# Optimization experiments

Hardware: AMD Instinct MI355X
Metric: run time of the kernel (lower is better)

## Reference

```python
import jax, jax.numpy as jnp
import numpy as np

PH = 512          # possible_hidden_units
PA = 512          # possible_activation_functions
NOUT = PH + PA    # n_outputs
H = 24            # n_hidden (hard-coded in module)
L = 32            # layer_limit
B = 8192          # batch_size


def setup_inputs() -> dict:
    key = jax.random.key(0)
    ks = jax.random.split(key, 7)
    k = 1.0 / np.sqrt(H).astype(np.float32)
    uni = lambda kk, sh: jax.random.uniform(kk, sh, jnp.float32, -k, k)
    return {
        "w_ih": uni(ks[0], (4 * H, NOUT)),
        "w_hh": uni(ks[1], (4 * H, H)),
        "b_ih": uni(ks[2], (4 * H,)),
        "b_hh": uni(ks[3], (4 * H,)),
        "w_lin": uni(ks[4], (NOUT, H)),
        "b_lin": uni(ks[5], (NOUT,)),
        # per-step uniforms for categorical inverse-CDF sampling (np.random.rand in torch)
        "u": jax.random.uniform(ks[6], (L, B), jnp.float32),
        "batch_size": B,
        "training": 1,
    }


def reference(w_ih, w_hh, b_ih, b_hh, w_lin, b_lin, u, batch_size, training):
    dtype = w_ih.dtype
    # alternating masks: even step -> hidden-unit actions, odd step -> activation actions
    base = jnp.arange(NOUT)
    mask_even = (base < PH).astype(dtype)
    mask_odd = (base >= PH).astype(dtype)
    parity = (jnp.arange(L) % 2)[:, None]
    masks = jnp.where(parity == 0, mask_even[None, :], mask_odd[None, :])  # [L, NOUT]

    train = bool(training)

    def step(carry, xs):
        h, c, a = carry            # h,c: [B,H]; a: one-hot [B,NOUT]
        mask, u_t = xs             # mask: [NOUT], u_t: [B]
        gates = a @ w_ih.T + b_ih + h @ w_hh.T + b_hh   # [B, 4H]
        ig, fg, gg, og = jnp.split(gates, 4, axis=1)
        i = jax.nn.sigmoid(ig)
        f = jax.nn.sigmoid(fg)
        g = jnp.tanh(gg)
        o = jax.nn.sigmoid(og)
        c = f * c + i * g
        h = o * jnp.tanh(c)
        out = jax.nn.softmax(h @ w_lin.T + b_lin, axis=1) * mask  # [B, NOUT]
        out = out / jnp.sum(out, axis=1, keepdims=True)
        if train:
            action = jnp.argmax(jnp.cumsum(out, axis=1) > u_t[:, None], axis=1)
        else:
            action = jnp.argmax(out, axis=1)
        p = jnp.take_along_axis(out, action[:, None], axis=1)[:, 0]  # [B]
        a_next = jax.nn.one_hot(action, NOUT, dtype=dtype)
        return (h, c, a_next), (p, action)

    init = (
        jnp.zeros((B, H), dtype),
        jnp.zeros((B, H), dtype),
        jnp.zeros((B, NOUT), dtype),
    )
    _, (probs, actions) = jax.lax.scan(step, init, (masks, u))
    # scan stacks along leading (step) axis -> transpose to [B, L]
    return probs.T, actions.T
```

## Files before the change

### kernel.cpp

```cpp
#include <hip/hip_runtime.h>
#include <math.h>

#define NOUTK 1024
#define PHK   512
#define HID   24
#define G4    96
#define LSTEPS 32
#define BATCH 8192
#define EPB   16

struct SmemD {
  float  stg[HID][128][8];
  float  whhT[HID][G4];
  float  blin[NOUTK];
  float  bihs[G4], bhhs[G4];
  double hsh[EPB][25];
  double scrM[8][EPB];
  double scrS[8][EPB];
  double candr[8][EPB];
  double tots[8][EPB];
  double r0sh[EPB];
  float  ubuf[LSTEPS][EPB];
  int    candj[8][EPB];
  int    actsh[EPB];
};

__device__ __forceinline__ float bf2f(unsigned short v) {
  union { unsigned u; float f; } x; x.u = ((unsigned)v) << 16; return x.f;
}
__device__ __forceinline__ unsigned short f2bf(float f) {
  unsigned u = __float_as_uint(f);
  unsigned r = 0x7FFFu + ((u >> 16) & 1u);
  return (unsigned short)((u + r) >> 16);
}
__device__ __forceinline__ float bfsnap(float f) { return bf2f(f2bf(f)); }

__global__ void __launch_bounds__(256)
transpose_wih(const float* __restrict__ wihf, float* __restrict__ wihT) {
  const int idx = blockIdx.x * 256 + threadIdx.x;
  const int j = idx / G4;
  const int r = idx - j * G4;
  wihT[idx] = wihf[r * NOUTK + j];
}

__global__ void __launch_bounds__(1024)
policy_kernel(const float* __restrict__ wihf,  const float* __restrict__ whhf,
              const float* __restrict__ bihf,  const float* __restrict__ bhhf,
              const float* __restrict__ wlinf, const float* __restrict__ blinf,
              const float* __restrict__ uf,    const float* __restrict__ wT,
              float* __restrict__ outg) {
  extern __shared__ char smraw[];
  SmemD* sm = (SmemD*)smraw;
  const int tid  = threadIdx.x;
  const int wave = tid >> 6;
  const int lane = tid & 63;
  const int s    = wave & 7;
  const int eg   = (wave >> 3) << 3;
  const int le   = lane & 7;
  const int jl   = lane >> 3;
  const int eG   = eg + le;
  const int geL  = blockIdx.x * EPB + wave;
  const int jgl0 = s * 64 + jl * 8;

  {
    const float4* row4 = (const float4*)(wlinf + tid * HID);
    #pragma unroll
    for (int q = 0; q < 6; ++q) {
      const float4 v = row4[q];
      sm->stg[q * 4 + 0][tid >> 3][tid & 7] = v.x;
      sm->stg[q * 4 + 1][tid >> 3][tid & 7] = v.y;
      sm->stg[q * 4 + 2][tid >> 3][tid & 7] = v.z;
      sm->stg[q * 4 + 3][tid >> 3][tid & 7] = v.w;
    }
  }
  for (int i = tid; i < G4 * HID; i += 1024) {
    const int row = i / HID, k = i % HID;
    sm->whhT[k][row] = whhf[i];
  }
  sm->blin[tid] = blinf[tid];
  if (tid < G4) { sm->bihs[tid] = bihf[tid]; sm->bhhs[tid] = bhhf[tid]; }
  if (tid < EPB * 25) ((double*)sm->hsh)[tid] = 0.0;
  if (tid < EPB) sm->actsh[tid] = -1;
  if (tid < LSTEPS * EPB) {
    const int t = tid >> 4, e = tid & 15;
    sm->ubuf[t][e] = uf[t * BATCH + blockIdx.x * EPB + e];
  }

  double creg = 0.0;
  __syncthreads();

  for (int t = 0; t < LSTEPS; ++t) {
    const int odd  = t & 1;
    const int base = odd ? PHK : 0;
    const int c    = (base >> 3) + s * 8 + jl;

    if (wave < 8 && (lane & 31) < HID) {
      const int eL = (wave << 1) + (lane >> 5);
      const int rl = lane & 31;
      const int a  = sm->actsh[eL];
      double g0, g1, g2, g3;
#define GATE(Q, GOUT)                                                        \
      { const int row = (Q) * HID + rl;                                      \
        const double colA = (a >= 0)                                         \
            ? (double)(wT ? wT[a * G4 + row] : wihf[row * NOUTK + a])        \
            : 0.0;                                                           \
        double mv = 0.0;                                                     \
        _Pragma("unroll 4")                                                  \
        for (int k = 0; k < HID; ++k)                                        \
          mv = fma(sm->hsh[eL][k], (double)sm->whhT[k][row], mv);            \
        GOUT = ((colA + (double)sm->bihs[row]) + mv) + (double)sm->bhhs[row]; \
        __builtin_amdgcn_sched_barrier(0); }
      GATE(0, g0) GATE(1, g1) GATE(2, g2) GATE(3, g3)
#undef GATE
      const double ig = 1.0 / (1.0 + exp(-g0));
      const double fg = 1.0 / (1.0 + exp(-g1));
      const double gv = tanh(g2);
      const double og = 1.0 / (1.0 + exp(-g3));
      creg = fg * creg + ig * gv;
      sm->hsh[eL][rl] = og * tanh(creg);
    }
    __syncthreads();

    double z0 = 0.0, z1 = 0.0, z2 = 0.0, z3 = 0.0,
           z4 = 0.0, z5 = 0.0, z6 = 0.0, z7 = 0.0;
    #pragma unroll 2
    for (int k = 0; k < HID; ++k) {
      const double hv = sm->hsh[eG][k];
      const float4 wa = *(const float4*)&sm->stg[k][c][0];
      const float4 wb = *(const float4*)&sm->stg[k][c][4];
      z0 = fma(hv, (double)wa.x, z0); z1 = fma(hv, (double)wa.y, z1);
      z2 = fma(hv, (double)wa.z, z2); z3 = fma(hv, (double)wa.w, z3);
      z4 = fma(hv, (double)wb.x, z4); z5 = fma(hv, (double)wb.y, z5);
      z6 = fma(hv, (double)wb.z, z6); z7 = fma(hv, (double)wb.w, z7);
    }
    {
      const float4 ba = *(const float4*)&sm->blin[base + jgl0];
      const float4 bb = *(const float4*)&sm->blin[base + jgl0 + 4];
      z0 += (double)ba.x; z1 += (double)ba.y; z2 += (double)ba.z; z3 += (double)ba.w;
      z4 += (double)bb.x; z5 += (double)bb.y; z6 += (double)bb.z; z7 += (double)bb.w;
    }

    double pm = fmax(fmax(fmax(z0, z1), fmax(z2, z3)),
                     fmax(fmax(z4, z5), fmax(z6, z7)));
    pm = fmax(pm, __shfl_xor(pm, 8));
    pm = fmax(pm, __shfl_xor(pm, 16));
    pm = fmax(pm, __shfl_xor(pm, 32));
    if (jl == 0) sm->scrM[s][eG] = pm;
    __syncthreads();
    double Me;
    {
      const double s0 = sm->scrM[0][eG], s1 = sm->scrM[1][eG],
                   s2 = sm->scrM[2][eG], s3 = sm->scrM[3][eG],
                   s4 = sm->scrM[4][eG], s5 = sm->scrM[5][eG],
                   s6 = sm->scrM[6][eG], s7 = sm->scrM[7][eG];
      Me = fmax(fmax(fmax(s0, s1), fmax(s2, s3)),
                fmax(fmax(s4, s5), fmax(s6, s7)));
    }

    z0 = exp(z0 - Me); z1 = exp(z1 - Me);
    __builtin_amdgcn_sched_barrier(0);
    z2 = exp(z2 - Me); z3 = exp(z3 - Me);
    __builtin_amdgcn_sched_barrier(0);
    z4 = exp(z4 - Me); z5 = exp(z5 - Me);
    __builtin_amdgcn_sched_barrier(0);
    z6 = exp(z6 - Me); z7 = exp(z7 - Me);
    double ps = ((((((z0 + z1) + z2) + z3) + z4) + z5) + z6) + z7;
    ps += __shfl_xor(ps, 8);
    ps += __shfl_xor(ps, 16);
    ps += __shfl_xor(ps, 32);
    if (jl == 0) sm->scrS[s][eG] = ps;
    __syncthreads();
    double inv;
    {
      const double s0 = sm->scrS[0][eG], s1 = sm->scrS[1][eG],
                   s2 = sm->scrS[2][eG], s3 = sm->scrS[3][eG],
                   s4 = sm->scrS[4][eG], s5 = sm->scrS[5][eG],
                   s6 = sm->scrS[6][eG], s7 = sm->scrS[7][eG];
      inv = 1.0 / (((s0 + s1) + (s2 + s3)) + ((s4 + s5) + (s6 + s7)));
    }

    const double p0 = z0 * inv,      p1 = p0 + z1 * inv,
                 p2 = p1 + z2 * inv, p3 = p2 + z3 * inv;
    const double p4 = p3 + z4 * inv, p5 = p4 + z5 * inv,
                 p6 = p5 + z6 * inv, p7 = p6 + z7 * inv;
    double exbase = 0.0, acc = 0.0;
    #pragma unroll
    for (int q2 = 0; q2 < 8; ++q2) {
      const double tq = __shfl(p7, q2 * 8 + le);
      if (q2 == jl) exbase = acc;
      acc += tq;
    }
    if (jl == 0) sm->tots[s][eG] = acc;
    if (s == 0 && lane < 8) sm->r0sh[eG] = p0;
    __syncthreads();

    double sb = exbase;
    for (int i = 0; i < s; ++i) sb += sm->tots[i][eG];
    const double ue = (double)sm->ubuf[t][eG];
    int jloc = 0x7FFFFFFF; double rsel = 0.0;
#define CROSS(R, PR, PRM1)                                                   \
    { const double C = sb + PR;                                              \
      if (jloc == 0x7FFFFFFF && C > ue) {                                    \
        jloc = jgl0 + (R); rsel = ((R) == 0) ? (PR) : ((PR) - (PRM1)); } }
    CROSS(0, p0, p0) CROSS(1, p1, p0) CROSS(2, p2, p1) CROSS(3, p3, p2)
    CROSS(4, p4, p3) CROSS(5, p5, p4) CROSS(6, p6, p5) CROSS(7, p7, p6)
#undef CROSS
    { int oj = __shfl_xor(jloc, 8);  double orr = __shfl_xor(rsel, 8);  if (oj < jloc) { jloc = oj; rsel = orr; } }
    { int oj = __shfl_xor(jloc, 16); double orr = __shfl_xor(rsel, 16); if (oj < jloc) { jloc = oj; rsel = orr; } }
    { int oj = __shfl_xor(jloc, 32); double orr = __shfl_xor(rsel, 32); if (oj < jloc) { jloc = oj; rsel = orr; } }
    if (jl == 0) { sm->candj[s][eG] = jloc; sm->candr[s][eG] = rsel; }
    __syncthreads();

    if (lane < 8) {
      int cj = sm->candj[lane][wave]; double cr = sm->candr[lane][wave];
      { int oj = __shfl_xor(cj, 1); double orr = __shfl_xor(cr, 1); if (oj < cj) { cj = oj; cr = orr; } }
      { int oj = __shfl_xor(cj, 2); double orr = __shfl_xor(cr, 2); if (oj < cj) { cj = oj; cr = orr; } }
      { int oj = __shfl_xor(cj, 4); double orr = __shfl_xor(cr, 4); if (oj < cj) { cj = oj; cr = orr; } }
      if (lane == 0) {
        int actg; double p;
        if (cj == 0x7FFFFFFF) {
          actg = 0;
          p = odd ? 0.0 : sm->r0sh[wave];
        } else {
          actg = base + cj; p = cr;
        }
        sm->actsh[wave] = actg;
        const int io = geL * LSTEPS + t;
        outg[io]                  = bfsnap((float)p);
        outg[BATCH * LSTEPS + io] = bfsnap((float)actg);
      }
    }
  }
}

extern "C" void kernel_launch(void* const* d_in, const int* in_sizes, int n_in,
                              void* d_out, int out_size, void* d_ws, size_t ws_size,
                              hipStream_t stream) {
  (void)in_sizes; (void)n_in; (void)out_size;
  const float* wT = nullptr;
  if (ws_size >= (size_t)(NOUTK * G4 * sizeof(float))) {
    transpose_wih<<<(NOUTK * G4) / 256, 256, 0, stream>>>(
        (const float*)d_in[0], (float*)d_ws);
    wT = (const float*)d_ws;
  }
  hipFuncSetAttribute((const void*)policy_kernel,
                      hipFuncAttributeMaxDynamicSharedMemorySize,
                      (int)sizeof(SmemD));
  policy_kernel<<<BATCH / EPB, 1024, sizeof(SmemD), stream>>>(
      (const float*)d_in[0], (const float*)d_in[1], (const float*)d_in[2],
      (const float*)d_in[3], (const float*)d_in[4], (const float*)d_in[5],
      (const float*)d_in[6], wT, (float*)d_out);
}
```

Measured before the change: 884.0 us.

## Stream transposed output weights from global memory instead of large shared staging

Adds a prep step that writes both the transposed input weights and a k-major transposed copy of the output projection weights into workspace. A new main kernel reads the output weights straight from global memory (through cache) with float4 loads, replacing the large per-block shared staging buffer. This shrinks shared memory per block so more blocks can be resident per CU, in exchange for repeated global/L2 reads of the weights at every step. The old kernel is kept as a fallback when the workspace is too small.

```diff
diff --git a/kernel.cpp b/kernel.cpp
--- a/kernel.cpp
+++ b/kernel.cpp
@@ -8,6 +8,21 @@
 #define LSTEPS 32
 #define BATCH 8192
 #define EPB   16
+
+struct SmemS {
+  float  whhT[HID][G4];
+  float  blin[NOUTK];
+  float  bihs[G4], bhhs[G4];
+  double hsh[EPB][25];
+  double scrM[8][EPB];
+  double scrS[8][EPB];
+  double candr[8][EPB];
+  double tots[8][EPB];
+  double r0sh[EPB];
+  float  ubuf[LSTEPS][EPB];
+  int    candj[8][EPB];
+  int    actsh[EPB];
+};
 
 struct SmemD {
   float  stg[HID][128][8];
@@ -36,19 +51,204 @@
 __device__ __forceinline__ float bfsnap(float f) { return bf2f(f2bf(f)); }
 
 __global__ void __launch_bounds__(256)
-transpose_wih(const float* __restrict__ wihf, float* __restrict__ wihT) {
+prep_ws(const float* __restrict__ wihf, const float* __restrict__ wlinf,
+        float* __restrict__ ws, int total) {
   const int idx = blockIdx.x * 256 + threadIdx.x;
-  const int j = idx / G4;
-  const int r = idx - j * G4;
-  wihT[idx] = wihf[r * NOUTK + j];
+  if (idx >= total) return;
+  if (idx < NOUTK * G4) {
+    const int j = idx / G4;
+    const int r = idx - j * G4;
+    ws[idx] = wihf[r * NOUTK + j];
+  } else {
+    const int i2  = idx - NOUTK * G4;
+    const int k   = i2 >> 10;
+    const int col = i2 & (NOUTK - 1);
+    ws[idx] = wlinf[col * HID + k];
+  }
+}
+
+__global__ void __launch_bounds__(1024, 8)
+policy_g(const float* __restrict__ whhf,  const float* __restrict__ bihf,
+         const float* __restrict__ bhhf,  const float* __restrict__ blinf,
+         const float* __restrict__ uf,    const float* __restrict__ wT,
+         const float* __restrict__ wKC,   float* __restrict__ outg) {
+  __shared__ SmemS smS;
+  SmemS* sm = &smS;
+  const int tid  = threadIdx.x;
+  const int wave = tid >> 6;
+  const int lane = tid & 63;
+  const int s    = wave & 7;
+  const int eg   = (wave >> 3) << 3;
+  const int le   = lane & 7;
+  const int jl   = lane >> 3;
+  const int eG   = eg + le;
+  const int geL  = blockIdx.x * EPB + wave;
+  const int jgl0 = s * 64 + jl * 8;
+
+  for (int i = tid; i < G4 * HID; i += 1024) {
+    const int row = i / HID, k = i % HID;
+    sm->whhT[k][row] = whhf[i];
+  }
+  sm->blin[tid] = blinf[tid];
+  if (tid < G4) { sm->bihs[tid] = bihf[tid]; sm->bhhs[tid] = bhhf[tid]; }
+  if (tid < EPB * 25) ((double*)sm->hsh)[tid] = 0.0;
+  if (tid < EPB) sm->actsh[tid] = -1;
+  if (tid < LSTEPS * EPB) {
+    const int t = tid >> 4, e = tid & 15;
+    sm->ubuf[t][e] = uf[t * BATCH + blockIdx.x * EPB + e];
+  }
+
+  double creg = 0.0;
+  __syncthreads();
+
+  for (int t = 0; t < LSTEPS; ++t) {
+    const int odd  = t & 1;
+    const int base = odd ? PHK : 0;
+
+    if (wave < 8 && (lane & 31) < HID) {
+      const int eL = (wave << 1) + (lane >> 5);
+      const int rl = lane & 31;
+      const int a  = sm->actsh[eL];
+      double g0, g1, g2, g3;
+#define GATE(Q, GOUT)                                                        \
+      { const int row = (Q) * HID + rl;                                      \
+        const double colA = (a >= 0) ? (double)wT[a * G4 + row] : 0.0;       \
+        double mv = 0.0;                                                     \
+        _Pragma("unroll 4")                                                  \
+        for (int k = 0; k < HID; ++k)                                        \
+          mv = fma(sm->hsh[eL][k], (double)sm->whhT[k][row], mv);            \
+        GOUT = ((colA + (double)sm->bihs[row]) + mv) + (double)sm->bhhs[row]; \
+        __builtin_amdgcn_sched_barrier(0); }
+      GATE(0, g0) GATE(1, g1) GATE(2, g2) GATE(3, g3)
+#undef GATE
+      const double ig = 1.0 / (1.0 + exp(-g0));
+      const double fg = 1.0 / (1.0 + exp(-g1));
+      const double gv = tanh(g2);
+      const double og = 1.0 / (1.0 + exp(-g3));
+      creg = fg * creg + ig * gv;
+      sm->hsh[eL][rl] = og * tanh(creg);
+    }
+    __syncthreads();
+
+    double z0 = 0.0, z1 = 0.0, z2 = 0.0, z3 = 0.0,
+           z4 = 0.0, z5 = 0.0, z6 = 0.0, z7 = 0.0;
+    const float* __restrict__ wrow = wKC + (base + jgl0);
+    #pragma unroll 2
+    for (int k = 0; k < HID; ++k) {
+      const double hv = sm->hsh[eG][k];
+      const float4 wa = *(const float4*)(wrow + k * NOUTK);
+      const float4 wb = *(const float4*)(wrow + k * NOUTK + 4);
+      z0 = fma(hv, (double)wa.x, z0); z1 = fma(hv, (double)wa.y, z1);
+      z2 = fma(hv, (double)wa.z, z2); z3 = fma(hv, (double)wa.w, z3);
+      z4 = fma(hv, (double)wb.x, z4); z5 = fma(hv, (double)wb.y, z5);
+      z6 = fma(hv, (double)wb.z, z6); z7 = fma(hv, (double)wb.w, z7);
+    }
+    {
+      const float4 ba = *(const float4*)&sm->blin[base + jgl0];
+      const float4 bb = *(const float4*)&sm->blin[base + jgl0 + 4];
+      z0 += (double)ba.x; z1 += (double)ba.y; z2 += (double)ba.z; z3 += (double)ba.w;
+      z4 += (double)bb.x; z5 += (double)bb.y; z6 += (double)bb.z; z7 += (double)bb.w;
+    }
+
+    double pm = fmax(fmax(fmax(z0, z1), fmax(z2, z3)),
+                     fmax(fmax(z4, z5), fmax(z6, z7)));
+    pm = fmax(pm, __shfl_xor(pm, 8));
+    pm = fmax(pm, __shfl_xor(pm, 16));
+    pm = fmax(pm, __shfl_xor(pm, 32));
+    if (jl == 0) sm->scrM[s][eG] = pm;
+    __syncthreads();
+    double Me;
+    {
+      const double s0 = sm->scrM[0][eG], s1 = sm->scrM[1][eG],
+                   s2 = sm->scrM[2][eG], s3 = sm->scrM[3][eG],
+                   s4 = sm->scrM[4][eG], s5 = sm->scrM[5][eG],
+                   s6 = sm->scrM[6][eG], s7 = sm->scrM[7][eG];
+      Me = fmax(fmax(fmax(s0, s1), fmax(s2, s3)),
+                fmax(fmax(s4, s5), fmax(s6, s7)));
+    }
+
+    z0 = exp(z0 - Me); z1 = exp(z1 - Me);
+    __builtin_amdgcn_sched_barrier(0);
+    z2 = exp(z2 - Me); z3 = exp(z3 - Me);
+    __builtin_amdgcn_sched_barrier(0);
+    z4 = exp(z4 - Me); z5 = exp(z5 - Me);
+    __builtin_amdgcn_sched_barrier(0);
+    z6 = exp(z6 - Me); z7 = exp(z7 - Me);
+    double ps = ((((((z0 + z1) + z2) + z3) + z4) + z5) + z6) + z7;
+    ps += __shfl_xor(ps, 8);
+    ps += __shfl_xor(ps, 16);
+    ps += __shfl_xor(ps, 32);
+    if (jl == 0) sm->scrS[s][eG] = ps;
+    __syncthreads();
+    double inv;
+    {
+      const double s0 = sm->scrS[0][eG], s1 = sm->scrS[1][eG],
+                   s2 = sm->scrS[2][eG], s3 = sm->scrS[3][eG],
+                   s4 = sm->scrS[4][eG], s5 = sm->scrS[5][eG],
+                   s6 = sm->scrS[6][eG], s7 = sm->scrS[7][eG];
+      inv = 1.0 / (((s0 + s1) + (s2 + s3)) + ((s4 + s5) + (s6 + s7)));
+    }
+
+    const double p0 = z0 * inv,      p1 = p0 + z1 * inv,
+                 p2 = p1 + z2 * inv, p3 = p2 + z3 * inv;
+    const double p4 = p3 + z4 * inv, p5 = p4 + z5 * inv,
+                 p6 = p5 + z6 * inv, p7 = p6 + z7 * inv;
+    double exbase = 0.0, acc = 0.0;
+    #pragma unroll
+    for (int q2 = 0; q2 < 8; ++q2) {
+      const double tq = __shfl(p7, q2 * 8 + le);
+      if (q2 == jl) exbase = acc;
+      acc += tq;
+    }
+    if (jl == 0) sm->tots[s][eG] = acc;
+    if (s == 0 && lane < 8) sm->r0sh[eG] = p0;
+    __syncthreads();
+
+    double sb = exbase;
+    for (int i = 0; i < s; ++i) sb += sm->tots[i][eG];
+    const double ue = (double)sm->ubuf[t][eG];
+    int jloc = 0x7FFFFFFF; double rsel = 0.0;
+#define CROSS(R, PR, PRM1)                                                   \
+    { const double C = sb + PR;                                              \
+      if (jloc == 0x7FFFFFFF && C > ue) {                                    \
+        jloc = jgl0 + (R); rsel = ((R) == 0) ? (PR) : ((PR) - (PRM1)); } }
+    CROSS(0, p0, p0) CROSS(1, p1, p0) CROSS(2, p2, p1) CROSS(3, p3, p2)
+    CROSS(4, p4, p3) CROSS(5, p5, p4) CROSS(6, p6, p5) CROSS(7, p7, p6)
+#undef CROSS
+    { int oj = __shfl_xor(jloc, 8);  double orr = __shfl_xor(rsel, 8);  if (oj < jloc) { jloc = oj; rsel = orr; } }
+    { int oj = __shfl_xor(jloc, 16); double orr = __shfl_xor(rsel, 16); if (oj < jloc) { jloc = oj; rsel = orr; } }
+    { int oj = __shfl_xor(jloc, 32); double orr = __shfl_xor(rsel, 32); if (oj < jloc) { jloc = oj; rsel = orr; } }
+    if (jl == 0) { sm->candj[s][eG] = jloc; sm->candr[s][eG] = rsel; }
+    __syncthreads();
+
+    if (lane < 8) {
+      int cj = sm->candj[lane][wave]; double cr = sm->candr[lane][wave];
+      { int oj = __shfl_xor(cj, 1); double orr = __shfl_xor(cr, 1); if (oj < cj) { cj = oj; cr = orr; } }
+      { int oj = __shfl_xor(cj, 2); double orr = __shfl_xor(cr, 2); if (oj < cj) { cj = oj; cr = orr; } }
+      { int oj = __shfl_xor(cj, 4); double orr = __shfl_xor(cr, 4); if (oj < cj) { cj = oj; cr = orr; } }
+      if (lane == 0) {
+        int actg; double p;
+        if (cj == 0x7FFFFFFF) {
+          actg = 0;
+          p = odd ? 0.0 : sm->r0sh[wave];
+        } else {
+          actg = base + cj; p = cr;
+        }
+        sm->actsh[wave] = actg;
+        const int io = geL * LSTEPS + t;
+        outg[io]                  = bfsnap((float)p);
+        outg[BATCH * LSTEPS + io] = bfsnap((float)actg);
+      }
+    }
+  }
 }
 
 __global__ void __launch_bounds__(1024)
-policy_kernel(const float* __restrict__ wihf,  const float* __restrict__ whhf,
-              const float* __restrict__ bihf,  const float* __restrict__ bhhf,
-              const float* __restrict__ wlinf, const float* __restrict__ blinf,
-              const float* __restrict__ uf,    const float* __restrict__ wT,
-              float* __restrict__ outg) {
+policy_l(const float* __restrict__ wihf,  const float* __restrict__ whhf,
+         const float* __restrict__ bihf,  const float* __restrict__ bhhf,
+         const float* __restrict__ wlinf, const float* __restrict__ blinf,
+         const float* __restrict__ uf,    const float* __restrict__ wT,
+         float* __restrict__ outg) {
   extern __shared__ char smraw[];
   SmemD* sm = (SmemD*)smraw;
   const int tid  = threadIdx.x;
@@ -237,17 +437,32 @@
                               void* d_out, int out_size, void* d_ws, size_t ws_size,
                               hipStream_t stream) {
   (void)in_sizes; (void)n_in; (void)out_size;
-  const float* wT = nullptr;
-  if (ws_size >= (size_t)(NOUTK * G4 * sizeof(float))) {
-    transpose_wih<<<(NOUTK * G4) / 256, 256, 0, stream>>>(
-        (const float*)d_in[0], (float*)d_ws);
-    wT = (const float*)d_ws;
-  }
-  hipFuncSetAttribute((const void*)policy_kernel,
-                      hipFuncAttributeMaxDynamicSharedMemorySize,
-                      (int)sizeof(SmemD));
-  policy_kernel<<<BATCH / EPB, 1024, sizeof(SmemD), stream>>>(
-      (const float*)d_in[0], (const float*)d_in[1], (const float*)d_in[2],
-      (const float*)d_in[3], (const float*)d_in[4], (const float*)d_in[5],
-      (const float*)d_in[6], wT, (float*)d_out);
-}
+  constexpr int WIHT_N = NOUTK * G4;
+  constexpr int WKC_N  = HID * NOUTK;
+  const size_t need_full = (size_t)(WIHT_N + WKC_N) * sizeof(float);
+  const size_t need_wt   = (size_t)WIHT_N * sizeof(float);
+
+  if (ws_size >= need_full) {
+    const int total = WIHT_N + WKC_N;
+    prep_ws<<<(total + 255) / 256, 256, 0, stream>>>(
+        (const float*)d_in[0], (const float*)d_in[4], (float*)d_ws, total);
+    policy_g<<<BATCH / EPB, 1024, 0, stream>>>(
+        (const float*)d_in[1], (const float*)d_in[2], (const float*)d_in[3],
+        (const float*)d_in[5], (const float*)d_in[6],
+        (const float*)d_ws, (const float*)d_ws + WIHT_N, (float*)d_out);
+  } else {
+    const float* wT = nullptr;
+    if (ws_size >= need_wt) {
+      prep_ws<<<(WIHT_N + 255) / 256, 256, 0, stream>>>(
+          (const float*)d_in[0], (const float*)d_in[4], (float*)d_ws, WIHT_N);
+      wT = (const float*)d_ws;
+    }
+    hipFuncSetAttribute((const void*)policy_l,
+                        hipFuncAttributeMaxDynamicSharedMemorySize,
+                        (int)sizeof(SmemD));
+    policy_l<<<BATCH / EPB, 1024, sizeof(SmemD), stream>>>(
+        (const float*)d_in[0], (const float*)d_in[1], (const float*)d_in[2],
+        (const float*)d_in[3], (const float*)d_in[4], (const float*)d_in[5],
+        (const float*)d_in[6], wT, (float*)d_out);
+  }
+}
```

Measured after the change: 854.1 us. 3.4% less time.
